# Kernel tuning notes

Measured on AMD Instinct MI355X. Metric: run time of the kernel, lower is better.

The kernel has to match this reference:

```python
import jax, jax.numpy as jnp
import numpy as np

N = 64      # bs_antenna_num
K = 16      # user_num
B = 8192    # batch
NOISE = 1.0 # noise_variance


def setup_inputs() -> dict:
    key = jax.random.key(0)
    k1, k2 = jax.random.split(key)
    H = jax.random.normal(k1, (B, N, K, 2), dtype=jnp.float32)
    P = jax.random.normal(k2, (B, 2 * N * K), dtype=jnp.float32)
    return {"H": H, "P": P}


def reference(H, P):
    b = H.shape[0]
    # transform_H: complex channel [B, N, K]
    Hc = jax.lax.complex(H[..., 0], H[..., 1])
    # recombine_P: complex precoder [B, N, K]
    Pr = P[:, : N * K].reshape(b, N, K)
    Pi = P[:, N * K :].reshape(b, N, K)
    Pc = jax.lax.complex(Pr, Pi)
    # plain (non-conjugated) dots, matching torch.matmul on complex vectors:
    # D[b,k,j] = sum_n H[b,n,k] * P[b,n,j]
    D = jnp.einsum('bnk,bnj->bkj', Hc, Pc)          # [B, K, K] complex
    mag2 = D.real ** 2 + D.imag ** 2                # |h_k . p_j|^2
    sig = jnp.diagonal(mag2, axis1=1, axis2=2)      # [B, K] desired signal
    total = mag2.sum(axis=2)                        # [B, K] total received
    interf = total - sig + NOISE                    # interference + noise
    rate = jnp.log2(1.0 + sig / interf).sum(axis=1) # per-sample sum-rate
    return -jnp.sum(rate) / b
```

## Files before the change

kernel.cpp:

```cpp
#include <hip/hip_runtime.h>


typedef short bf16x8 __attribute__((ext_vector_type(8)));
typedef float f32x4  __attribute__((ext_vector_type(4)));
typedef int   i32x4  __attribute__((ext_vector_type(4)));

__device__ __forceinline__ int pk2(float lo, float hi) {
    int r;
    asm("v_cvt_pk_bf16_f32 %0, %1, %2" : "=v"(r) : "v"(lo), "v"(hi));
    return r;
}

__device__ __forceinline__ bf16x8 mk8(const float* v) {
    i32x4 t;
    #pragma unroll
    for (int i = 0; i < 4; ++i) t[i] = pk2(v[2 * i], v[2 * i + 1]);
    return __builtin_bit_cast(bf16x8, t);
}

__device__ __forceinline__ bf16x8 negbf(bf16x8 a) {
    i32x4 t = __builtin_bit_cast(i32x4, a);
    #pragma unroll
    for (int i = 0; i < 4; ++i) t[i] ^= 0x80008000;
    return __builtin_bit_cast(bf16x8, t);
}

__device__ __forceinline__ void gload16(const float* g, float* s) {
    __builtin_amdgcn_global_load_lds(
        (const __attribute__((address_space(1))) void*)g,
        (__attribute__((address_space(3))) void*)s,
        16, 0, 0);
}

#define MFMA __builtin_amdgcn_mfma_f32_16x16x32_bf16

__global__ __launch_bounds__(256, 4) void sumrate_kernel(
        const float* __restrict__ H, const float* __restrict__ P,
        float* __restrict__ ws) {
    __shared__ float sP[4 * 2048];
    __shared__ float sRate[4];

    const int wave = threadIdx.x >> 6;
    const int lane = threadIdx.x & 63;
    const int b    = blockIdx.x * 4 + wave;
    const int j    = lane & 15;
    const int g    = lane >> 4;
    const int n0   = g * 8;

    const float* gP = P + (size_t)b * 2048;
    const float* hA = H + (size_t)b * 2048 + n0 * 32 + 2 * j;
    float* sPw = sP + wave * 2048;

    #pragma unroll
    for (int i = 0; i < 8; ++i)
        gload16(gP + i * 256 + lane * 4, sPw + i * 256);

    float2 h0[8], h1[8];
    #pragma unroll
    for (int r = 0; r < 8; ++r) {
        h0[r] = *reinterpret_cast<const float2*>(hA + r * 32);
        h1[r] = *reinterpret_cast<const float2*>(hA + 1024 + r * 32);
    }
    __builtin_amdgcn_sched_barrier(0);

    float ar0[8], ai0[8], ar1[8], ai1[8];
    #pragma unroll
    for (int r = 0; r < 8; ++r) {
        ar0[r] = h0[r].x; ai0[r] = h0[r].y;
        ar1[r] = h1[r].x; ai1[r] = h1[r].y;
    }
    const bf16x8 Ahr0 = mk8(ar0), Ahr1 = mk8(ar1);
    const bf16x8 Ahi0 = mk8(ai0), Ahi1 = mk8(ai1);

    asm volatile("s_waitcnt vmcnt(0)" ::: "memory");
    __builtin_amdgcn_sched_barrier(0);

    float pr0[8], pr1[8], pi0[8], pi1[8];
    #pragma unroll
    for (int r = 0; r < 8; ++r) {
        pr0[r] = sPw[(n0 + r) * 16 + j];
        pr1[r] = sPw[(n0 + r + 32) * 16 + j];
        pi0[r] = sPw[1024 + (n0 + r) * 16 + j];
        pi1[r] = sPw[1024 + (n0 + r + 32) * 16 + j];
    }
    const bf16x8 Bpr0 = mk8(pr0), Bpr1 = mk8(pr1);
    const bf16x8 Bpi0 = mk8(pi0), Bpi1 = mk8(pi1);

    f32x4 dr = {0.f, 0.f, 0.f, 0.f}, di = {0.f, 0.f, 0.f, 0.f};
    dr = MFMA(Ahr0, Bpr0, dr, 0, 0, 0);
    dr = MFMA(Ahr1, Bpr1, dr, 0, 0, 0);
    dr = MFMA(negbf(Ahi0), Bpi0, dr, 0, 0, 0);
    dr = MFMA(negbf(Ahi1), Bpi1, dr, 0, 0, 0);
    di = MFMA(Ahr0, Bpi0, di, 0, 0, 0);
    di = MFMA(Ahr1, Bpi1, di, 0, 0, 0);
    di = MFMA(Ahi0, Bpr0, di, 0, 0, 0);
    di = MFMA(Ahi1, Bpr1, di, 0, 0, 0);

    float tot[4], sig[4];
    #pragma unroll
    for (int r = 0; r < 4; ++r) {
        const float mag = dr[r] * dr[r] + di[r] * di[r];
        const int k = g * 4 + r;
        tot[r] = mag;
        sig[r] = (j == k) ? mag : 0.0f;
    }
    #pragma unroll
    for (int m = 1; m < 16; m <<= 1) {
        #pragma unroll
        for (int r = 0; r < 4; ++r) {
            tot[r] += __shfl_xor(tot[r], m, 64);
            sig[r] += __shfl_xor(sig[r], m, 64);
        }
    }
    float rate = 0.0f;
    #pragma unroll
    for (int r = 0; r < 4; ++r)
        rate += log2f(1.0f + sig[r] / (tot[r] - sig[r] + 1.0f));
    rate += __shfl_xor(rate, 16, 64);
    rate += __shfl_xor(rate, 32, 64);

    if (lane == 0) sRate[wave] = rate;
    __syncthreads();
    if (threadIdx.x == 0)
        ws[blockIdx.x] = sRate[0] + sRate[1] + sRate[2] + sRate[3];
}

__global__ __launch_bounds__(1024) void reduce_kernel(
        const float* __restrict__ ws, float* __restrict__ out) {
    __shared__ float sPart[16];
    float s = ws[threadIdx.x] + ws[threadIdx.x + 1024];

    #pragma unroll
    for (int m = 1; m < 64; m <<= 1)
        s += __shfl_xor(s, m, 64);

    const int w = threadIdx.x >> 6;
    const int l = threadIdx.x & 63;
    if (l == 0) sPart[w] = s;
    __syncthreads();

    if (w == 0) {
        float t = (l < 16) ? sPart[l] : 0.0f;
        #pragma unroll
        for (int m = 1; m < 16; m <<= 1)
            t += __shfl_xor(t, m, 64);
        if (l == 0) out[0] = t * (-1.0f / 8192.0f);
    }
}

extern "C" void kernel_launch(void* const* d_in, const int* in_sizes, int n_in,
                              void* d_out, int out_size, void* d_ws, size_t ws_size,
                              hipStream_t stream) {
    const float* H = (const float*)d_in[0];
    const float* P = (const float*)d_in[1];
    float* out = (float*)d_out;
    float* ws  = (float*)d_ws;

    sumrate_kernel<<<8192 / 4, 256, 0, stream>>>(H, P, ws);
    reduce_kernel<<<1, 1024, 0, stream>>>(ws, out);
}
```

Measured before the change: 27.12 us.

## Double-buffer H and P through LDS with persistent waves handling eight batches

Each wave now loops over eight consecutive batch samples instead of one. Both H and P are staged into a per-wave double-buffered LDS region with async global-to-LDS loads, so the next sample's fetch overlaps the current sample's MFMA and reduction work. The grid shrinks to 512 blocks of two waves, and each wave writes its partial sum straight to the workspace, which removes the block-level barrier. The kernel was already close to memory-bandwidth bound, and with only about four waves per CU and a two-deep pipeline there may be too few loads in flight to keep HBM saturated.

```diff
diff --git a/kernel.cpp b/kernel.cpp
--- a/kernel.cpp
+++ b/kernel.cpp
@@ -34,55 +34,37 @@
 
 #define MFMA __builtin_amdgcn_mfma_f32_16x16x32_bf16
 
-__global__ __launch_bounds__(256, 4) void sumrate_kernel(
-        const float* __restrict__ H, const float* __restrict__ P,
-        float* __restrict__ ws) {
-    __shared__ float sP[4 * 2048];
-    __shared__ float sRate[4];
+__device__ __forceinline__ void stage(const float* gH, const float* gP,
+                                      float* dst, int lane) {
+    #pragma unroll
+    for (int ii = 0; ii < 8; ++ii)
+        gload16(gH + ii * 256 + lane * 4, dst + ii * 256);
+    #pragma unroll
+    for (int ii = 0; ii < 8; ++ii)
+        gload16(gP + ii * 256 + lane * 4, dst + 2048 + ii * 256);
+}
 
-    const int wave = threadIdx.x >> 6;
-    const int lane = threadIdx.x & 63;
-    const int b    = blockIdx.x * 4 + wave;
-    const int j    = lane & 15;
-    const int g    = lane >> 4;
-    const int n0   = g * 8;
-
-    const float* gP = P + (size_t)b * 2048;
-    const float* hA = H + (size_t)b * 2048 + n0 * 32 + 2 * j;
-    float* sPw = sP + wave * 2048;
-
-    #pragma unroll
-    for (int i = 0; i < 8; ++i)
-        gload16(gP + i * 256 + lane * 4, sPw + i * 256);
-
-    float2 h0[8], h1[8];
-    #pragma unroll
-    for (int r = 0; r < 8; ++r) {
-        h0[r] = *reinterpret_cast<const float2*>(hA + r * 32);
-        h1[r] = *reinterpret_cast<const float2*>(hA + 1024 + r * 32);
-    }
-    __builtin_amdgcn_sched_barrier(0);
-
+__device__ __forceinline__ float computeBatch(const float* buf,
+                                              int j, int g, int n0) {
     float ar0[8], ai0[8], ar1[8], ai1[8];
     #pragma unroll
     for (int r = 0; r < 8; ++r) {
-        ar0[r] = h0[r].x; ai0[r] = h0[r].y;
-        ar1[r] = h1[r].x; ai1[r] = h1[r].y;
+        const float2 h0 = *reinterpret_cast<const float2*>(buf + (n0 + r) * 32 + 2 * j);
+        const float2 h1 = *reinterpret_cast<const float2*>(buf + (n0 + r + 32) * 32 + 2 * j);
+        ar0[r] = h0.x; ai0[r] = h0.y;
+        ar1[r] = h1.x; ai1[r] = h1.y;
+    }
+    const float* bp = buf + 2048;
+    float pr0[8], pr1[8], pi0[8], pi1[8];
+    #pragma unroll
+    for (int r = 0; r < 8; ++r) {
+        pr0[r] = bp[(n0 + r) * 16 + j];
+        pr1[r] = bp[(n0 + r + 32) * 16 + j];
+        pi0[r] = bp[1024 + (n0 + r) * 16 + j];
+        pi1[r] = bp[1024 + (n0 + r + 32) * 16 + j];
     }
     const bf16x8 Ahr0 = mk8(ar0), Ahr1 = mk8(ar1);
     const bf16x8 Ahi0 = mk8(ai0), Ahi1 = mk8(ai1);
-
-    asm volatile("s_waitcnt vmcnt(0)" ::: "memory");
-    __builtin_amdgcn_sched_barrier(0);
-
-    float pr0[8], pr1[8], pi0[8], pi1[8];
-    #pragma unroll
-    for (int r = 0; r < 8; ++r) {
-        pr0[r] = sPw[(n0 + r) * 16 + j];
-        pr1[r] = sPw[(n0 + r + 32) * 16 + j];
-        pi0[r] = sPw[1024 + (n0 + r) * 16 + j];
-        pi1[r] = sPw[1024 + (n0 + r + 32) * 16 + j];
-    }
     const bf16x8 Bpr0 = mk8(pr0), Bpr1 = mk8(pr1);
     const bf16x8 Bpi0 = mk8(pi0), Bpi1 = mk8(pi1);
 
@@ -118,17 +100,46 @@
         rate += log2f(1.0f + sig[r] / (tot[r] - sig[r] + 1.0f));
     rate += __shfl_xor(rate, 16, 64);
     rate += __shfl_xor(rate, 32, 64);
+    return rate;
+}
 
-    if (lane == 0) sRate[wave] = rate;
-    __syncthreads();
-    if (threadIdx.x == 0)
-        ws[blockIdx.x] = sRate[0] + sRate[1] + sRate[2] + sRate[3];
+__global__ __launch_bounds__(128, 1) void sumrate_kernel(
+        const float* __restrict__ H, const float* __restrict__ P,
+        float* __restrict__ ws) {
+    __shared__ float sBuf[2][2][4096];
+
+    const int w    = threadIdx.x >> 6;
+    const int lane = threadIdx.x & 63;
+    const int gw   = blockIdx.x * 2 + w;
+    const int j    = lane & 15;
+    const int g    = lane >> 4;
+    const int n0   = g * 8;
+
+    const float* gH = H + (size_t)gw * 8 * 2048;
+    const float* gP = P + (size_t)gw * 8 * 2048;
+
+    stage(gH, gP, &sBuf[w][0][0], lane);
+
+    float rateAcc = 0.0f;
+    #pragma unroll
+    for (int i = 0; i < 8; ++i) {
+        if (i < 7)
+            stage(gH + (i + 1) * 2048, gP + (i + 1) * 2048,
+                  &sBuf[w][(i + 1) & 1][0], lane);
+        if (i < 7) asm volatile("s_waitcnt vmcnt(16)" ::: "memory");
+        else       asm volatile("s_waitcnt vmcnt(0)"  ::: "memory");
+        __builtin_amdgcn_sched_barrier(0);
+        rateAcc += computeBatch(&sBuf[w][i & 1][0], j, g, n0);
+        __builtin_amdgcn_sched_barrier(0);
+    }
+
+    if (lane == 0) ws[gw] = rateAcc;
 }
 
 __global__ __launch_bounds__(1024) void reduce_kernel(
         const float* __restrict__ ws, float* __restrict__ out) {
     __shared__ float sPart[16];
-    float s = ws[threadIdx.x] + ws[threadIdx.x + 1024];
+    float s = ws[threadIdx.x];
 
     #pragma unroll
     for (int m = 1; m < 64; m <<= 1)
@@ -156,6 +167,6 @@
     float* out = (float*)d_out;
     float* ws  = (float*)d_ws;
 
-    sumrate_kernel<<<8192 / 4, 256, 0, stream>>>(H, P, ws);
+    sumrate_kernel<<<512, 128, 0, stream>>>(H, P, ws);
     reduce_kernel<<<1, 1024, 0, stream>>>(ws, out);
 }
```

After: 30.38 us. +12.0%, slower.
